# Kernel optimization log

Hardware: AMD Instinct MI355X
Metric: run time of the kernel (lower is better)

## Reference

```python
import jax, jax.numpy as jnp
import numpy as np

DIM = 128
KS = 7
HEADS = 4
HEAD_DIM = DIM // HEADS


def setup_inputs() -> dict:
    key = jax.random.key(0)
    ks = jax.random.split(key, 10)
    B, H, W, C = 4, 64, 64, DIM
    s = 0.02
    return {
        "x": jax.random.normal(ks[0], (B, H, W, C), jnp.float32),
        "qkv_w": jax.random.normal(ks[1], (C, 3 * C), jnp.float32) * s,
        "qkv_b": jnp.zeros((3 * C,), jnp.float32),
        "proj_w": jax.random.normal(ks[2], (C, C), jnp.float32) * s,
        "proj_b": jnp.zeros((C,), jnp.float32),
        "rpb": jax.random.normal(ks[3], (HEADS, 2 * KS - 1, 2 * KS - 1), jnp.float32) * s,
        "g1_w": jax.random.normal(ks[4], (C, C // 2), jnp.float32) * s,
        "g1_b": jnp.zeros((C // 2,), jnp.float32),
        "g2_w": jax.random.normal(ks[5], (C // 2, 1), jnp.float32) * s,
        "g2_b": jnp.zeros((1,), jnp.float32),
    }


def _neighborhood_attention(x, qkv_w, qkv_b, proj_w, proj_b, rpb):
    B, H, W, C = x.shape
    k = KS
    # qkv projection -> [B,H,W,3,heads,head_dim]
    qkv = (x @ qkv_w + qkv_b).reshape(B, H, W, 3, HEADS, HEAD_DIM)
    q = qkv[..., 0, :, :] * (HEAD_DIM ** -0.5)  # [B,H,W,h,d]
    kk = qkv[..., 1, :, :]
    v = qkv[..., 2, :, :]

    # Clamped sliding-window start indices (NATTEN semantics)
    sh = jnp.clip(jnp.arange(H) - k // 2, 0, H - k)  # [H]
    sw = jnp.clip(jnp.arange(W) - k // 2, 0, W - k)  # [W]
    idx_h = sh[:, None] + jnp.arange(k)[None, :]  # [H,k]
    idx_w = sw[:, None] + jnp.arange(k)[None, :]  # [W,k]

    # Gather neighborhood windows: [B,H,W,k,k,h,d]
    kwin = kk[:, idx_h[:, None, :, None], idx_w[None, :, None, :]]
    vwin = v[:, idx_h[:, None, :, None], idx_w[None, :, None, :]]

    # Relative position bias indices: (neighbor - query) + (k-1)
    bih = idx_h - jnp.arange(H)[:, None] + (k - 1)  # [H,k]
    biw = idx_w - jnp.arange(W)[:, None] + (k - 1)  # [W,k]
    # bias: [h,H,W,k,k] -> [H,W,h,k,k]
    bias = rpb[:, bih[:, None, :, None], biw[None, :, None, :]]
    bias = jnp.transpose(bias, (1, 2, 0, 3, 4))

    # scores: [B,H,W,h,k,k]
    scores = jnp.einsum('bxyhd,bxyklhd->bxyhkl', q, kwin) + bias[None]
    attn = jax.nn.softmax(scores.reshape(B, H, W, HEADS, k * k), axis=-1)
    attn = attn.reshape(B, H, W, HEADS, k, k)
    out = jnp.einsum('bxyhkl,bxyklhd->bxyhd', attn, vwin).reshape(B, H, W, C)
    return out @ proj_w + proj_b


def reference(x, qkv_w, qkv_b, proj_w, proj_b, rpb, g1_w, g1_b, g2_w, g2_b):
    attn_out = _neighborhood_attention(x, qkv_w, qkv_b, proj_w, proj_b, rpb)
    gate = jax.nn.sigmoid(jax.nn.relu(x @ g1_w + g1_b) @ g2_w + g2_b)  # [B,H,W,1]
    return attn_out * gate + x
```

## Files before the change

kernel.cpp:

```cpp
#include <hip/hip_runtime.h>
#include <hip/hip_bf16.h>
#include <math.h>

#define PIXELS 16384
#define C      128
#define KS     7
#define HEADS  4
#define HD     32
#define QSCALE 0.17677669529663687f

typedef __bf16 bf16x8 __attribute__((ext_vector_type(8)));
typedef float  f32x4  __attribute__((ext_vector_type(4)));

__device__ inline unsigned short f2bf(float f) {
    unsigned int u = __builtin_bit_cast(unsigned int, f);
    u += 0x7FFFu + ((u >> 16) & 1u);
    return (unsigned short)(u >> 16);
}
__device__ inline float bflo(unsigned int u) {
    return __builtin_bit_cast(float, u << 16);
}
__device__ inline float bfhi(unsigned int u) {
    return __builtin_bit_cast(float, u & 0xFFFF0000u);
}

__global__ __launch_bounds__(256) void prep_kernel(
    const float* __restrict__ qkv_w, const float* __restrict__ g1_w,
    const float* __restrict__ qkv_b, const float* __restrict__ g1_b,
    const float* __restrict__ proj_w,
    unsigned short* __restrict__ wT, unsigned short* __restrict__ pT,
    float* __restrict__ bias_ext)
{
    const int blk = blockIdx.x, tid = threadIdx.x;
    if (blk < 56) {
        int n = blk * 8 + (tid >> 5);
        int kq = tid & 31;
        float f0, f1, f2, f3;
        if (n < 384) {
            f0 = qkv_w[(kq*4+0)*384 + n]; f1 = qkv_w[(kq*4+1)*384 + n];
            f2 = qkv_w[(kq*4+2)*384 + n]; f3 = qkv_w[(kq*4+3)*384 + n];
        } else {
            int nn = n - 384;
            f0 = g1_w[(kq*4+0)*64 + nn]; f1 = g1_w[(kq*4+1)*64 + nn];
            f2 = g1_w[(kq*4+2)*64 + nn]; f3 = g1_w[(kq*4+3)*64 + nn];
        }
        ushort4 o; o.x = f2bf(f0); o.y = f2bf(f1); o.z = f2bf(f2); o.w = f2bf(f3);
        *(ushort4*)(wT + n*128 + kq*4) = o;
    } else if (blk < 72) {
        int n = (blk - 56) * 8 + (tid >> 5);
        int kq = tid & 31;
        ushort4 o;
        o.x = f2bf(proj_w[(kq*4+0)*128 + n]);
        o.y = f2bf(proj_w[(kq*4+1)*128 + n]);
        o.z = f2bf(proj_w[(kq*4+2)*128 + n]);
        o.w = f2bf(proj_w[(kq*4+3)*128 + n]);
        *(ushort4*)(pT + n*128 + kq*4) = o;
    } else {
        for (int idx = tid; idx < 448; idx += 256)
            bias_ext[idx] = (idx < 384) ? qkv_b[idx] : g1_b[idx - 384];
    }
}

__global__ __launch_bounds__(256) void gemm_qkvh_fused(
    const float* __restrict__ x, const unsigned short* __restrict__ wT,
    const float* __restrict__ bias_ext, const float* __restrict__ g2_w,
    const float* __restrict__ g2_b, unsigned short* __restrict__ qkvb,
    float* __restrict__ gate)
{
    __shared__ __align__(16) unsigned short As[64*128];
    __shared__ __align__(16) unsigned short Bs[64*128];
    const int nt = blockIdx.x;
    const int n0 = nt * 64;
    const int m0 = blockIdx.y * 64;
    const int tid = threadIdx.x;

#pragma unroll
    for (int it = 0; it < 4; it++) {
        int idx = tid + it*256, row = idx >> 4, c = idx & 15;
        const float* src = x + (size_t)(m0+row)*128 + c*8;
        float4 a = *(const float4*)src;
        float4 b2 = *(const float4*)(src + 4);
        uint4 v;
        v.x = (unsigned int)f2bf(a.x)  | ((unsigned int)f2bf(a.y)  << 16);
        v.y = (unsigned int)f2bf(a.z)  | ((unsigned int)f2bf(a.w)  << 16);
        v.z = (unsigned int)f2bf(b2.x) | ((unsigned int)f2bf(b2.y) << 16);
        v.w = (unsigned int)f2bf(b2.z) | ((unsigned int)f2bf(b2.w) << 16);
        *(uint4*)(As + row*128 + ((c ^ (row&7)) << 3)) = v;
    }
#pragma unroll
    for (int it = 0; it < 4; it++) {
        int idx = tid + it*256, row = idx >> 4, c = idx & 15;
        uint4 v = *(const uint4*)(wT + (size_t)(n0+row)*128 + c*8);
        *(uint4*)(Bs + row*128 + ((c ^ (row&7)) << 3)) = v;
    }
    __syncthreads();

    const int wave = tid >> 6, lane = tid & 63;
    const int l15 = lane & 15, quad = lane >> 4;
    const int wm = (wave & 1) * 32, wn = (wave >> 1) * 32;

    f32x4 acc[2][2] = {};
#pragma unroll
    for (int ks = 0; ks < 4; ks++) {
        bf16x8 af[2], bq[2];
#pragma unroll
        for (int mt = 0; mt < 2; mt++) {
            int m = wm + mt*16 + l15;
            af[mt] = *(const bf16x8*)(As + m*128 + (((ks*4+quad) ^ (m&7)) << 3));
        }
#pragma unroll
        for (int ntl = 0; ntl < 2; ntl++) {
            int n = wn + ntl*16 + l15;
            bq[ntl] = *(const bf16x8*)(Bs + n*128 + (((ks*4+quad) ^ (n&7)) << 3));
        }
#pragma unroll
        for (int mt = 0; mt < 2; mt++)
#pragma unroll
            for (int ntl = 0; ntl < 2; ntl++)
                acc[mt][ntl] = __builtin_amdgcn_mfma_f32_16x16x32_bf16(
                    af[mt], bq[ntl], acc[mt][ntl], 0, 0, 0);
    }
    __syncthreads();

    if (nt < 6) {
        unsigned short* Cs = (unsigned short*)As;
#pragma unroll
        for (int ntl = 0; ntl < 2; ntl++) {
            int nl = wn + ntl*16 + l15;
            int ng = n0 + nl;
            float qs = (ng < 128) ? QSCALE : 1.0f;
            float bv = bias_ext[ng];
#pragma unroll
            for (int mt = 0; mt < 2; mt++)
#pragma unroll
                for (int r = 0; r < 4; r++) {
                    int ml = wm + mt*16 + quad*4 + r;
                    Cs[ml*64 + nl] = f2bf((acc[mt][ntl][r] + bv) * qs);
                }
        }
        __syncthreads();
        int row = tid >> 2, part = tid & 3;
        uint4 a = *(const uint4*)(Cs + row*64 + part*16);
        uint4 b = *(const uint4*)(Cs + row*64 + part*16 + 8);
        unsigned short* dst = qkvb + (size_t)(m0+row)*384 + n0 + part*16;
        *(uint4*)dst = a;
        *(uint4*)(dst + 8) = b;
    } else {
        float* gpart = (float*)Bs;
        float rs[2][4];
#pragma unroll
        for (int mt = 0; mt < 2; mt++)
#pragma unroll
            for (int r = 0; r < 4; r++) rs[mt][r] = 0.0f;
#pragma unroll
        for (int ntl = 0; ntl < 2; ntl++) {
            int nl = wn + ntl*16 + l15;
            float bv = bias_ext[384 + nl];
            float gw = g2_w[nl];
#pragma unroll
            for (int mt = 0; mt < 2; mt++)
#pragma unroll
                for (int r = 0; r < 4; r++) {
                    float h = acc[mt][ntl][r] + bv;
                    rs[mt][r] += fmaxf(h, 0.0f) * gw;
                }
        }
#pragma unroll
        for (int off = 1; off <= 8; off <<= 1)
#pragma unroll
            for (int mt = 0; mt < 2; mt++)
#pragma unroll
                for (int r = 0; r < 4; r++)
                    rs[mt][r] += __shfl_xor(rs[mt][r], off);
        if (l15 == 0) {
#pragma unroll
            for (int mt = 0; mt < 2; mt++)
#pragma unroll
                for (int r = 0; r < 4; r++)
                    gpart[(wave >> 1)*64 + wm + mt*16 + quad*4 + r] = rs[mt][r];
        }
        __syncthreads();
        if (tid < 64) {
            float g = gpart[tid] + gpart[64 + tid] + g2_b[0];
            gate[m0 + tid] = 1.0f / (1.0f + __expf(-g));
        }
    }
}

__global__ __launch_bounds__(128) void attn_kernel(
    const unsigned short* __restrict__ qkvb, const float* __restrict__ rpb,
    unsigned short* __restrict__ attnb)
{
    __shared__ __align__(16) unsigned short kvs[196 * 136];
    __shared__ float rpb_lds[2 * 169];

    const int blk = blockIdx.x;
    const int pr = blk & 1;
    const int tile = (blk >> 1) & 63;
    const int b = blk >> 7;
    const int ti0 = (tile >> 3) * 8, tj0 = (tile & 7) * 8;
    int wr0 = ti0 - 3; if (wr0 < 0) wr0 = 0;
    int wc0 = tj0 - 3; if (wc0 < 0) wc0 = 0;

    const int tid = threadIdx.x;

    for (int t = tid; t < 338; t += 128) rpb_lds[t] = rpb[pr * 338 + t];

    for (int idx = tid; idx < 196 * 16; idx += 128) {
        int pos = idx >> 4, t = idx & 15;
        int wr = pos / 14, wc = pos - wr * 14;
        int gr = wr0 + wr; if (gr > 63) gr = 63;
        int gc = wc0 + wc; if (gc > 63) gc = 63;
        size_t gp = (size_t)(((b << 6) + gr) << 6) + gc;
        int src = 128 + ((t >> 3) << 7) + pr * 64 + ((t & 7) << 3);
        uint4 v = *(const uint4*)(qkvb + gp * 384 + src);
        *(uint4*)(kvs + pos * 136 + ((t >> 3) << 6) + ((t & 7) << 3)) = v;
    }
    __syncthreads();

    const int hh = tid >> 6, lane = tid & 63;
    const int h = pr * 2 + hh;
    const int pi = lane >> 3, pj = lane & 7;
    const int i = ti0 + pi, j = tj0 + pj;
    int sh = i - 3; sh = sh < 0 ? 0 : (sh > 57 ? 57 : sh);
    int sw = j - 3; sw = sw < 0 ? 0 : (sw > 57 ? 57 : sw);
    const int dr = sh - wr0, dc = sw - wc0;
    const size_t gp = (size_t)(((b << 6) + i) << 6) + j;

    unsigned int qu[16];
    const unsigned short* qptr = qkvb + gp * 384 + h * 32;
    *(uint4*)(qu + 0)  = *(const uint4*)(qptr + 0);
    *(uint4*)(qu + 4)  = *(const uint4*)(qptr + 8);
    *(uint4*)(qu + 8)  = *(const uint4*)(qptr + 16);
    *(uint4*)(qu + 12) = *(const uint4*)(qptr + 24);
    float qf[32];
#pragma unroll
    for (int p = 0; p < 16; p++) {
        qf[2*p]   = bflo(qu[p]);
        qf[2*p+1] = bfhi(qu[p]);
    }

    float acc[32];
#pragma unroll
    for (int d = 0; d < 32; d++) acc[d] = 0.0f;
    float ssum = 0.0f;

    const float* rl = rpb_lds + hh * 169;
    const int rbase = (sh - i + 6) * 13 + (sw - j + 6);
    const int hwbase = (dr * 14 + dc) * 136 + hh * 32;

    for (int kr = 0; kr < 7; kr++) {
        int hw = hwbase + kr * (14 * 136);
        int ri = rbase + kr * 13;
#pragma unroll
        for (int kc = 0; kc < 7; kc++) {
            const unsigned short* kp = kvs + hw;
            unsigned int ku[16];
            *(uint4*)(ku + 0)  = *(const uint4*)(kp + 0);
            *(uint4*)(ku + 4)  = *(const uint4*)(kp + 8);
            *(uint4*)(ku + 8)  = *(const uint4*)(kp + 16);
            *(uint4*)(ku + 12) = *(const uint4*)(kp + 24);
            float s0 = rl[ri + kc], s1 = 0.0f;
#pragma unroll
            for (int p = 0; p < 8; p++) {
                s0 += qf[2*p]      * bflo(ku[p])     + qf[2*p+1]  * bfhi(ku[p]);
                s1 += qf[2*p+16]   * bflo(ku[p+8])   + qf[2*p+17] * bfhi(ku[p+8]);
            }
            float e = __expf(s0 + s1);
            ssum += e;
            unsigned int vu[16];
            *(uint4*)(vu + 0)  = *(const uint4*)(kp + 64);
            *(uint4*)(vu + 4)  = *(const uint4*)(kp + 72);
            *(uint4*)(vu + 8)  = *(const uint4*)(kp + 80);
            *(uint4*)(vu + 12) = *(const uint4*)(kp + 88);
#pragma unroll
            for (int p = 0; p < 16; p++) {
                acc[2*p]   += e * bflo(vu[p]);
                acc[2*p+1] += e * bfhi(vu[p]);
            }
            hw += 136;
        }
    }

    const float inv = 1.0f / ssum;
    unsigned int o[16];
#pragma unroll
    for (int p = 0; p < 16; p++) {
        unsigned int lo = f2bf(acc[2*p] * inv);
        unsigned int hi = f2bf(acc[2*p+1] * inv);
        o[p] = lo | (hi << 16);
    }
    unsigned short* op = attnb + gp * 128 + h * 32;
    *(uint4*)(op + 0)  = *(const uint4*)(o + 0);
    *(uint4*)(op + 8)  = *(const uint4*)(o + 4);
    *(uint4*)(op + 16) = *(const uint4*)(o + 8);
    *(uint4*)(op + 24) = *(const uint4*)(o + 12);
}

__global__ __launch_bounds__(256) void gemm_proj_mfma(
    const unsigned short* __restrict__ ab, const unsigned short* __restrict__ pT,
    const float* __restrict__ proj_b, const float* __restrict__ gate,
    const float* __restrict__ x, float* __restrict__ out)
{
    __shared__ __align__(16) unsigned short As[64*128];
    __shared__ __align__(16) unsigned short Bs[64*128];
    const int n0 = blockIdx.x * 64;
    const int m0 = blockIdx.y * 64;
    const int tid = threadIdx.x;

#pragma unroll
    for (int it = 0; it < 4; it++) {
        int idx = tid + it*256, row = idx >> 4, c = idx & 15;
        uint4 v = *(const uint4*)(ab + (size_t)(m0+row)*128 + c*8);
        *(uint4*)(As + row*128 + ((c ^ (row&7)) << 3)) = v;
    }
#pragma unroll
    for (int it = 0; it < 4; it++) {
        int idx = tid + it*256, row = idx >> 4, c = idx & 15;
        uint4 v = *(const uint4*)(pT + (size_t)(n0+row)*128 + c*8);
        *(uint4*)(Bs + row*128 + ((c ^ (row&7)) << 3)) = v;
    }
    __syncthreads();

    const int wave = tid >> 6, lane = tid & 63;
    const int l15 = lane & 15, quad = lane >> 4;
    const int wm = (wave & 1) * 32, wn = (wave >> 1) * 32;

    f32x4 acc[2][2] = {};
#pragma unroll
    for (int ks = 0; ks < 4; ks++) {
        bf16x8 af[2], bq[2];
#pragma unroll
        for (int mt = 0; mt < 2; mt++) {
            int m = wm + mt*16 + l15;
            af[mt] = *(const bf16x8*)(As + m*128 + (((ks*4+quad) ^ (m&7)) << 3));
        }
#pragma unroll
        for (int ntl = 0; ntl < 2; ntl++) {
            int n = wn + ntl*16 + l15;
            bq[ntl] = *(const bf16x8*)(Bs + n*128 + (((ks*4+quad) ^ (n&7)) << 3));
        }
#pragma unroll
        for (int mt = 0; mt < 2; mt++)
#pragma unroll
            for (int ntl = 0; ntl < 2; ntl++)
                acc[mt][ntl] = __builtin_amdgcn_mfma_f32_16x16x32_bf16(
                    af[mt], bq[ntl], acc[mt][ntl], 0, 0, 0);
    }
    __syncthreads();

    float* Cs = (float*)As;
#pragma unroll
    for (int ntl = 0; ntl < 2; ntl++) {
        int nl = wn + ntl*16 + l15;
        float bv = proj_b[n0 + nl];
#pragma unroll
        for (int mt = 0; mt < 2; mt++)
#pragma unroll
            for (int r = 0; r < 4; r++) {
                int ml = wm + mt*16 + quad*4 + r;
                Cs[ml*64 + nl] = acc[mt][ntl][r] + bv;
            }
    }
    __syncthreads();
    int row = tid >> 2, part = tid & 3;
    float gv = gate[m0 + row];
    const float* xr = x + (size_t)(m0+row)*128 + n0 + part*16;
    float* orow = out + (size_t)(m0+row)*128 + n0 + part*16;
#pragma unroll
    for (int q = 0; q < 4; q++) {
        float4 cv = *(const float4*)(Cs + row*64 + part*16 + q*4);
        float4 xv = *(const float4*)(xr + q*4);
        float4 o;
        o.x = cv.x * gv + xv.x; o.y = cv.y * gv + xv.y;
        o.z = cv.z * gv + xv.z; o.w = cv.w * gv + xv.w;
        *(float4*)(orow + q*4) = o;
    }
}

extern "C" void kernel_launch(void* const* d_in, const int* in_sizes, int n_in,
                              void* d_out, int out_size, void* d_ws, size_t ws_size,
                              hipStream_t stream)
{
    const float* x      = (const float*)d_in[0];
    const float* qkv_w  = (const float*)d_in[1];
    const float* qkv_b  = (const float*)d_in[2];
    const float* proj_w = (const float*)d_in[3];
    const float* proj_b = (const float*)d_in[4];
    const float* rpb    = (const float*)d_in[5];
    const float* g1_w   = (const float*)d_in[6];
    const float* g1_b   = (const float*)d_in[7];
    const float* g2_w   = (const float*)d_in[8];
    const float* g2_b   = (const float*)d_in[9];
    float* out = (float*)d_out;

    float* ws        = (float*)d_ws;
    float* gate      = ws;
    float* bias_ext  = gate + 16384;
    unsigned short* wT    = (unsigned short*)(bias_ext + 448);
    unsigned short* pT    = wT + 57344;
    unsigned short* qkvb  = pT + 16384;
    unsigned short* attnb = qkvb + 6291456;

    (void)in_sizes; (void)n_in; (void)out_size; (void)ws_size;

    prep_kernel<<<73, 256, 0, stream>>>(qkv_w, g1_w, qkv_b, g1_b, proj_w,
                                        wT, pT, bias_ext);
    gemm_qkvh_fused<<<dim3(7, 256), 256, 0, stream>>>(x, wT, bias_ext,
                                                      g2_w, g2_b, qkvb, gate);
    attn_kernel<<<512, 128, 0, stream>>>(qkvb, rpb, attnb);
    gemm_proj_mfma<<<dim3(2, 256), 256, 0, stream>>>(attnb, pT, proj_b, gate, x, out);
}
```

Measured before the change: 126.2 us.

## Split attention blocks per head and use bf16 dot2 for QK scores

The attention kernel now launches one 64-thread block per head and 8x8 tile instead of one 128-thread block per head pair, so shared memory per block halves and the grid grows fourfold. This is meant to raise occupancy and parallelism on the MI355X. The QK dot product now uses the fdot2 bf16 builtin on packed q and k words instead of unpacking q to fp32 and doing scalar FMAs, which cuts instruction count and register use. In exchange the grid has more blocks and fewer waves per block, and fdot2 may differ slightly in rounding.

```diff
diff --git a/kernel.cpp b/kernel.cpp
--- a/kernel.cpp
+++ b/kernel.cpp
@@ -10,6 +10,7 @@
 #define QSCALE 0.17677669529663687f
 
 typedef __bf16 bf16x8 __attribute__((ext_vector_type(8)));
+typedef __bf16 bf16x2 __attribute__((ext_vector_type(2)));
 typedef float  f32x4  __attribute__((ext_vector_type(4)));
 
 __device__ inline unsigned short f2bf(float f) {
@@ -187,39 +188,38 @@
     }
 }
 
-__global__ __launch_bounds__(128) void attn_kernel(
+__global__ __launch_bounds__(64) void attn_kernel(
     const unsigned short* __restrict__ qkvb, const float* __restrict__ rpb,
     unsigned short* __restrict__ attnb)
 {
-    __shared__ __align__(16) unsigned short kvs[196 * 136];
-    __shared__ float rpb_lds[2 * 169];
+    __shared__ __align__(16) unsigned short kvs[196 * 68];
+    __shared__ float rpb_lds[169];
 
     const int blk = blockIdx.x;
-    const int pr = blk & 1;
-    const int tile = (blk >> 1) & 63;
-    const int b = blk >> 7;
-    const int ti0 = (tile >> 3) * 8, tj0 = (tile & 7) * 8;
+    const int h = blk & 3;
+    const int tile = (blk >> 2) & 63;
+    const int b = blk >> 8;
+    const int ti0 = ((tile >> 3) << 3), tj0 = ((tile & 7) << 3);
     int wr0 = ti0 - 3; if (wr0 < 0) wr0 = 0;
     int wc0 = tj0 - 3; if (wc0 < 0) wc0 = 0;
 
     const int tid = threadIdx.x;
 
-    for (int t = tid; t < 338; t += 128) rpb_lds[t] = rpb[pr * 338 + t];
-
-    for (int idx = tid; idx < 196 * 16; idx += 128) {
-        int pos = idx >> 4, t = idx & 15;
+    for (int t = tid; t < 169; t += 64) rpb_lds[t] = rpb[h * 169 + t];
+
+    for (int idx = tid; idx < 196 * 8; idx += 64) {
+        int pos = idx >> 3, t = idx & 7;
         int wr = pos / 14, wc = pos - wr * 14;
         int gr = wr0 + wr; if (gr > 63) gr = 63;
         int gc = wc0 + wc; if (gc > 63) gc = 63;
         size_t gp = (size_t)(((b << 6) + gr) << 6) + gc;
-        int src = 128 + ((t >> 3) << 7) + pr * 64 + ((t & 7) << 3);
+        int src = 128 + ((t >> 2) << 7) + h * 32 + ((t & 3) << 3);
         uint4 v = *(const uint4*)(qkvb + gp * 384 + src);
-        *(uint4*)(kvs + pos * 136 + ((t >> 3) << 6) + ((t & 7) << 3)) = v;
-    }
-    __syncthreads();
-
-    const int hh = tid >> 6, lane = tid & 63;
-    const int h = pr * 2 + hh;
+        *(uint4*)(kvs + pos * 68 + ((t >> 2) << 5) + ((t & 3) << 3)) = v;
+    }
+    __syncthreads();
+
+    const int lane = tid;
     const int pi = lane >> 3, pj = lane & 7;
     const int i = ti0 + pi, j = tj0 + pj;
     int sh = i - 3; sh = sh < 0 ? 0 : (sh > 57 ? 57 : sh);
@@ -233,52 +233,50 @@
     *(uint4*)(qu + 4)  = *(const uint4*)(qptr + 8);
     *(uint4*)(qu + 8)  = *(const uint4*)(qptr + 16);
     *(uint4*)(qu + 12) = *(const uint4*)(qptr + 24);
-    float qf[32];
-#pragma unroll
-    for (int p = 0; p < 16; p++) {
-        qf[2*p]   = bflo(qu[p]);
-        qf[2*p+1] = bfhi(qu[p]);
-    }
 
     float acc[32];
 #pragma unroll
     for (int d = 0; d < 32; d++) acc[d] = 0.0f;
     float ssum = 0.0f;
 
-    const float* rl = rpb_lds + hh * 169;
     const int rbase = (sh - i + 6) * 13 + (sw - j + 6);
-    const int hwbase = (dr * 14 + dc) * 136 + hh * 32;
+    const int hwbase = (dr * 14 + dc) * 68;
 
     for (int kr = 0; kr < 7; kr++) {
-        int hw = hwbase + kr * (14 * 136);
-        int ri = rbase + kr * 13;
+        const unsigned short* rowp = kvs + hwbase + kr * (14 * 68);
+        const float* rl = rpb_lds + rbase + kr * 13;
 #pragma unroll
         for (int kc = 0; kc < 7; kc++) {
-            const unsigned short* kp = kvs + hw;
+            const unsigned short* kp = rowp + kc * 68;
             unsigned int ku[16];
             *(uint4*)(ku + 0)  = *(const uint4*)(kp + 0);
             *(uint4*)(ku + 4)  = *(const uint4*)(kp + 8);
             *(uint4*)(ku + 8)  = *(const uint4*)(kp + 16);
             *(uint4*)(ku + 12) = *(const uint4*)(kp + 24);
-            float s0 = rl[ri + kc], s1 = 0.0f;
-#pragma unroll
-            for (int p = 0; p < 8; p++) {
-                s0 += qf[2*p]      * bflo(ku[p])     + qf[2*p+1]  * bfhi(ku[p]);
-                s1 += qf[2*p+16]   * bflo(ku[p+8])   + qf[2*p+17] * bfhi(ku[p+8]);
-            }
-            float e = __expf(s0 + s1);
+            float s = rl[kc];
+#if __has_builtin(__builtin_amdgcn_fdot2_f32_bf16)
+#pragma unroll
+            for (int p = 0; p < 16; p++)
+                s = __builtin_amdgcn_fdot2_f32_bf16(
+                        __builtin_bit_cast(bf16x2, qu[p]),
+                        __builtin_bit_cast(bf16x2, ku[p]), s, false);
+#else
+#pragma unroll
+            for (int p = 0; p < 16; p++)
+                s += bflo(qu[p]) * bflo(ku[p]) + bfhi(qu[p]) * bfhi(ku[p]);
+#endif
+            float e = __expf(s);
             ssum += e;
             unsigned int vu[16];
-            *(uint4*)(vu + 0)  = *(const uint4*)(kp + 64);
-            *(uint4*)(vu + 4)  = *(const uint4*)(kp + 72);
-            *(uint4*)(vu + 8)  = *(const uint4*)(kp + 80);
-            *(uint4*)(vu + 12) = *(const uint4*)(kp + 88);
+            *(uint4*)(vu + 0)  = *(const uint4*)(kp + 32);
+            *(uint4*)(vu + 4)  = *(const uint4*)(kp + 40);
+            *(uint4*)(vu + 8)  = *(const uint4*)(kp + 48);
+            *(uint4*)(vu + 12) = *(const uint4*)(kp + 56);
 #pragma unroll
             for (int p = 0; p < 16; p++) {
                 acc[2*p]   += e * bflo(vu[p]);
                 acc[2*p+1] += e * bfhi(vu[p]);
             }
-            hw += 136;
         }
     }
 
@@ -408,6 +406,6 @@
                                         wT, pT, bias_ext);
     gemm_qkvh_fused<<<dim3(7, 256), 256, 0, stream>>>(x, wT, bias_ext,
                                                       g2_w, g2_b, qkvb, gate);
-    attn_kernel<<<512, 128, 0, stream>>>(qkvb, rpb, attnb);
+    attn_kernel<<<2048, 64, 0, stream>>>(qkvb, rpb, attnb);
     gemm_proj_mfma<<<dim3(2, 256), 256, 0, stream>>>(attnb, pT, proj_b, gate, x, out);
 }
```

New measurement: 215.9 us. 1.71x slower.
